# Kernel tuning notes

Measured on AMD Instinct MI355X. Metric: run time of the kernel, lower is better.

## Reference

```python
import jax, jax.numpy as jnp
import numpy as np

B, N, C = 2, 2048, 256
L, H = 4, 4
HD = C // H  # 64, div=1 so q/k keep full head dim
EPS = 1e-5   # BatchNorm eps (eval mode, running_mean=0, running_var=1)


def setup_inputs() -> dict:
    key = jax.random.key(0)
    ks = jax.random.split(key, 20)
    w = lambda k, s: jax.random.normal(k, s, jnp.float32) * 0.05
    return {
        'x': jax.random.normal(ks[0], (B, N, C), jnp.float32),
        'in_w1': w(ks[1], (C, C)), 'in_b1': w(ks[2], (C,)),
        'in_g1': 1.0 + w(ks[3], (C,)), 'in_be1': w(ks[4], (C,)),
        'in_w2': w(ks[5], (C, C)), 'in_b2': w(ks[6], (C,)),
        'in_g2': 1.0 + w(ks[7], (C,)), 'in_be2': w(ks[8], (C,)),
        'q_w': w(ks[9], (L, H, HD, HD)), 'k_w': w(ks[10], (L, H, HD, HD)),
        'v_w': w(ks[11], (L, H, HD, HD)), 'v_b': w(ks[12], (L, H, HD)),
        't_w': w(ks[13], (L, H, HD, HD)), 't_b': w(ks[14], (L, H, HD)),
        'bn_g': 1.0 + w(ks[15], (L, H, HD)), 'bn_b': w(ks[16], (L, H, HD)),
        'proj_w': w(ks[17], (L, C, C)), 'proj_b': w(ks[18], (L, C)),
    }


def _bn(t, g, b):
    # eval-mode BatchNorm1d with running_mean=0, running_var=1
    return t * (g / jnp.sqrt(1.0 + EPS))[:, None] + b[:, None]


def _forward(x, in_w1, in_b1, in_g1, in_be1, in_w2, in_b2, in_g2, in_be2,
             q_w, k_w, v_w, v_b, t_w, t_b, bn_g, bn_b, proj_w, proj_b):
    Bq, Nq, Cq = x.shape
    h = x.transpose(0, 2, 1)  # (B, C, N)
    h = jax.nn.relu(_bn(jnp.einsum('oc,bcn->bon', in_w1, h) + in_b1[:, None], in_g1, in_be1))
    h = jax.nn.relu(_bn(jnp.einsum('oc,bcn->bon', in_w2, h) + in_b2[:, None], in_g2, in_be2))
    h = h.reshape(Bq, H, HD, Nq)  # split heads (B, H, hd, N)
    for l in range(L):
        xq = jnp.einsum('hoc,bhcn->bhno', q_w[l], h)                       # (B,H,N,hd)
        xk = jnp.einsum('hoc,bhcn->bhon', k_w[l], h)                       # (B,H,hd,N)
        xv = jnp.einsum('hoc,bhcn->bhon', v_w[l], h) + v_b[l][None, :, :, None]
        attn = jax.nn.softmax(jnp.einsum('bhno,bhom->bhnm', xq, xk), axis=-1)
        # offset-attention normalization: divide by column sums (torch dim=1)
        attn = attn / (1e-9 + attn.sum(axis=2, keepdims=True))
        xr = jnp.einsum('bhcn,bhnm->bhcm', xv, attn)                       # (B,H,hd,N)
        d = h - xr
        t = jnp.einsum('hoc,bhcn->bhon', t_w[l], d) + t_b[l][None, :, :, None]
        xr = jax.nn.relu(t * (bn_g[l] / jnp.sqrt(1.0 + EPS))[None, :, :, None]
                         + bn_b[l][None, :, :, None])
        h = h + xr
        hm = h.reshape(Bq, Cq, Nq)  # concat heads
        hm = jnp.einsum('oc,bcn->bon', proj_w[l], hm) + proj_b[l][:, None]
        h = hm.reshape(Bq, H, HD, Nq)
    return h.reshape(Bq, Cq, Nq).transpose(0, 2, 1)  # (B, N, C)


def reference(x, in_w1, in_b1, in_g1, in_be1, in_w2, in_b2, in_g2, in_be2,
              q_w, k_w, v_w, v_b, t_w, t_b, bn_g, bn_b, proj_w, proj_b):
    return _forward(x, in_w1, in_b1, in_g1, in_be1, in_w2, in_b2, in_g2, in_be2,
                    q_w, k_w, v_w, v_b, t_w, t_b, bn_g, bn_b, proj_w, proj_b)
```

## Files before the change

kernel.cpp:

```cpp
#include <hip/hip_runtime.h>
#include <math.h>

constexpr int NB = 2, NN = 2048, NC = 256, NL = 4, NH = 4, ND = 64;
constexpr float EPSV = 1e-5f;

using half8 = __attribute__((ext_vector_type(8))) _Float16;
using half4 = __attribute__((ext_vector_type(4))) _Float16;
using f32x4 = __attribute__((ext_vector_type(4))) float;

__device__ __forceinline__ f32x4 mfma16(half8 a, half8 b, f32x4 c) {
    return __builtin_amdgcn_mfma_f32_16x16x32_f16(a, b, c, 0, 0, 0);
}
__device__ __forceinline__ half8 cvt8(const float* p) {
    float4 x0 = *(const float4*)p, x1 = *(const float4*)(p + 4);
    half8 h;
    h[0]=(_Float16)x0.x; h[1]=(_Float16)x0.y; h[2]=(_Float16)x0.z; h[3]=(_Float16)x0.w;
    h[4]=(_Float16)x1.x; h[5]=(_Float16)x1.y; h[6]=(_Float16)x1.z; h[7]=(_Float16)x1.w;
    return h;
}

template<int EPI, bool INF16, bool OUT32>
__global__ __launch_bounds__(256) void gemm_mfma(
    const float* __restrict__ Wg, const float* __restrict__ bias,
    const float* __restrict__ gam, const float* __restrict__ bet,
    const void* __restrict__ inp, void* __restrict__ outp)
{
    int b = blockIdx.x, o0 = blockIdx.y * 64, n0 = blockIdx.z * 32;
    int t = threadIdx.x, w = t >> 6, li = t & 15, qd = (t >> 4) & 3;
    const float* wr = Wg + (size_t)(o0 + w * 16 + li) * NC + qd * 8;
    half8 af[8];
#pragma unroll
    for (int ks = 0; ks < 8; ++ks) af[ks] = cvt8(wr + ks * 32);
    f32x4 acc[2];
    acc[0] = {0.f, 0.f, 0.f, 0.f}; acc[1] = {0.f, 0.f, 0.f, 0.f};
#pragma unroll
    for (int ks = 0; ks < 8; ++ks) {
#pragma unroll
        for (int g = 0; g < 2; ++g) {
            int n = n0 + g * 16 + li;
            half8 bf;
            if (INF16) {
                bf = *(const half8*)((const _Float16*)inp +
                        ((size_t)(b * NN + n) * NC + ks * 32 + qd * 8));
            } else {
                bf = cvt8((const float*)inp + ((size_t)(b * NN + n) * NC + ks * 32 + qd * 8));
            }
            acc[g] = mfma16(af[ks], bf, acc[g]);
        }
    }
    int ob = o0 + w * 16 + qd * 4;
    float4 bs = *(const float4*)(bias + ob);
    float4 gs = {0,0,0,0}, be = {0,0,0,0};
    if (EPI == 1) { gs = *(const float4*)(gam + ob); be = *(const float4*)(bet + ob); }
    float scl = rsqrtf(1.f + EPSV);
#pragma unroll
    for (int g = 0; g < 2; ++g) {
        int n = n0 + g * 16 + li;
        float v4[4];
#pragma unroll
        for (int r = 0; r < 4; ++r) {
            float v = acc[g][r] + ((const float*)&bs)[r];
            if (EPI == 1)
                v = fmaxf(0.f, v * (((const float*)&gs)[r] * scl) + ((const float*)&be)[r]);
            v4[r] = v;
        }
        if (OUT32) {
            float4 fv = {v4[0], v4[1], v4[2], v4[3]};
            *(float4*)((float*)outp + (size_t)(b * NN + n) * NC + ob) = fv;
        } else {
            half4 hv;
#pragma unroll
            for (int r = 0; r < 4; ++r) hv[r] = (_Float16)v4[r];
            *(half4*)((_Float16*)outp + (size_t)(b * NN + n) * NC + ob) = hv;
        }
    }
}

__global__ __launch_bounds__(256) void qkv_fused(
    const float* __restrict__ qw, const float* __restrict__ kw,
    const float* __restrict__ vw, const float* __restrict__ vb,
    const _Float16* __restrict__ h16, _Float16* __restrict__ q16,
    _Float16* __restrict__ k16, _Float16* __restrict__ v16, int l)
{
    int bh = blockIdx.x, n0 = blockIdx.y * 64;
    int hh = bh & 3, b = bh >> 2;
    size_t wbase = (size_t)(l * NH + hh) * ND * ND;
    int t = threadIdx.x, w = t >> 6, li = t & 15, qd = (t >> 4) & 3;
    size_t wro = (size_t)(w * 16 + li) * ND + qd * 8;
    half8 aq0 = cvt8(qw + wbase + wro), aq1 = cvt8(qw + wbase + wro + 32);
    half8 ak0 = cvt8(kw + wbase + wro), ak1 = cvt8(kw + wbase + wro + 32);
    half8 av0 = cvt8(vw + wbase + wro), av1 = cvt8(vw + wbase + wro + 32);
    f32x4 accq[4], acck[4], accv[4];
#pragma unroll
    for (int g = 0; g < 4; ++g) {
        accq[g] = {0.f,0.f,0.f,0.f}; acck[g] = {0.f,0.f,0.f,0.f}; accv[g] = {0.f,0.f,0.f,0.f};
    }
#pragma unroll
    for (int g = 0; g < 4; ++g) {
        int n = n0 + g * 16 + li;
        const _Float16* hb = h16 + ((size_t)(b * NN + n) * NC + hh * 64 + qd * 8);
        half8 b0 = *(const half8*)(hb);
        half8 b1 = *(const half8*)(hb + 32);
        accq[g] = mfma16(aq0, b0, accq[g]); accq[g] = mfma16(aq1, b1, accq[g]);
        acck[g] = mfma16(ak0, b0, acck[g]); acck[g] = mfma16(ak1, b1, acck[g]);
        accv[g] = mfma16(av0, b0, accv[g]); accv[g] = mfma16(av1, b1, accv[g]);
    }
    int ob = w * 16 + qd * 4;
    _Float16* qo = q16 + (size_t)bh * NN * ND;
    _Float16* ko = k16 + (size_t)bh * NN * ND;
#pragma unroll
    for (int g = 0; g < 4; ++g) {
        int n = n0 + g * 16 + li;
        half4 hq, hk;
#pragma unroll
        for (int r = 0; r < 4; ++r) { hq[r] = (_Float16)accq[g][r]; hk[r] = (_Float16)acck[g][r]; }
        *(half4*)(qo + (size_t)n * ND + ob) = hq;
        *(half4*)(ko + (size_t)n * ND + ob) = hk;
    }
    float4 vb4 = *(const float4*)(vb + (size_t)(l * NH + hh) * ND + ob);
    _Float16* vo = v16 + (size_t)bh * ND * NN;
#pragma unroll
    for (int g = 0; g < 4; ++g) {
        int n = n0 + g * 16 + li;
#pragma unroll
        for (int r = 0; r < 4; ++r)
            vo[(size_t)(ob + r) * NN + n] = (_Float16)(accv[g][r] + ((const float*)&vb4)[r]);
    }
}

__global__ __launch_bounds__(256) void rowsum_part(
    const _Float16* __restrict__ qh, const _Float16* __restrict__ kh,
    float* __restrict__ rowsum_p)
{
    int bh = blockIdx.x, nt = blockIdx.y, ms = blockIdx.z;
    const _Float16* qp = qh + (size_t)bh * NN * ND;
    const _Float16* kp = kh + (size_t)bh * NN * ND;
    int t = threadIdx.x, w = t >> 6, li = t & 15, qd = (t >> 4) & 3;
    int nr = nt * 64 + w * 16;
    half8 aq0 = *(const half8*)(qp + (size_t)(nr + li) * ND + qd * 8);
    half8 aq1 = *(const half8*)(qp + (size_t)(nr + li) * ND + qd * 8 + 32);
    float rsacc[4] = {0.f, 0.f, 0.f, 0.f};
    for (int it = 0; it < 8; ++it) {
        int m0 = ms * 512 + it * 64;
        f32x4 s[4];
#pragma unroll
        for (int g = 0; g < 4; ++g) {
            const _Float16* kb = kp + (size_t)(m0 + g * 16 + li) * ND + qd * 8;
            half8 b0 = *(const half8*)(kb);
            half8 b1 = *(const half8*)(kb + 32);
            s[g] = {0.f, 0.f, 0.f, 0.f};
            s[g] = mfma16(aq0, b0, s[g]);
            s[g] = mfma16(aq1, b1, s[g]);
        }
#pragma unroll
        for (int r = 0; r < 4; ++r)
            rsacc[r] += __expf(s[0][r]) + __expf(s[1][r]) + __expf(s[2][r]) + __expf(s[3][r]);
    }
#pragma unroll
    for (int r = 0; r < 4; ++r) {
        float v = rsacc[r];
        v += __shfl_xor(v, 1); v += __shfl_xor(v, 2);
        v += __shfl_xor(v, 4); v += __shfl_xor(v, 8);
        if (li == 0) rowsum_p[((size_t)(ms * NB * NH + bh)) * NN + nr + qd * 4 + r] = v;
    }
}

__global__ __launch_bounds__(256) void attn_part(
    const _Float16* __restrict__ qh, const _Float16* __restrict__ kh,
    const _Float16* __restrict__ vh, const float* __restrict__ rowsum_p,
    _Float16* __restrict__ xrp16, float* __restrict__ csp)
{
    int bh = blockIdx.x, m0 = blockIdx.y * 64, ns = blockIdx.z;
    const _Float16* qp = qh + (size_t)bh * NN * ND;
    const _Float16* kp = kh + (size_t)bh * NN * ND;
    const _Float16* vp = vh + (size_t)bh * ND * NN;
    __shared__ __align__(16) _Float16 Plds[2][64 * 72];
    __shared__ float cs_wave[4][64];
    int t = threadIdx.x, w = t >> 6, li = t & 15, qd = (t >> 4) & 3;
    const size_t RSS = (size_t)NB * NH * NN;
    half8 bk[4][2];
#pragma unroll
    for (int g = 0; g < 4; ++g) {
        const _Float16* kb = kp + (size_t)(m0 + g * 16 + li) * ND + qd * 8;
        bk[g][0] = *(const half8*)(kb);
        bk[g][1] = *(const half8*)(kb + 32);
    }
    f32x4 acc[4];
#pragma unroll
    for (int g = 0; g < 4; ++g) acc[g] = {0.f, 0.f, 0.f, 0.f};
    float csacc[4] = {0.f, 0.f, 0.f, 0.f};
    int nb0 = ns * 512;
    const _Float16* qrow0 = qp + (size_t)(nb0 + w * 16 + li) * ND + qd * 8;
    half8 aq0 = *(const half8*)(qrow0);
    half8 aq1 = *(const half8*)(qrow0 + 32);
    int ridx = bh * NN + nb0 + w * 16 + qd * 4;
    float4 r0 = *(const float4*)(rowsum_p + ridx);
    float4 r1 = *(const float4*)(rowsum_p + RSS + ridx);
    float4 r2 = *(const float4*)(rowsum_p + 2 * RSS + ridx);
    float4 r3 = *(const float4*)(rowsum_p + 3 * RSS + ridx);
    for (int it = 0; it < 8; ++it) {
        int n0 = ns * 512 + it * 64;
        _Float16* Pb = Plds[it & 1];
        const _Float16* vrow = vp + (size_t)(w * 16 + li) * NN + n0 + qd * 8;
        half8 av0 = *(const half8*)(vrow);
        half8 av1 = *(const half8*)(vrow + 32);
        f32x4 s[4];
#pragma unroll
        for (int g = 0; g < 4; ++g) {
            s[g] = {0.f, 0.f, 0.f, 0.f};
            s[g] = mfma16(aq0, bk[g][0], s[g]);
            s[g] = mfma16(aq1, bk[g][1], s[g]);
        }
        float irs[4];
        irs[0] = 1.f / (r0.x + r1.x + r2.x + r3.x);
        irs[1] = 1.f / (r0.y + r1.y + r2.y + r3.y);
        irs[2] = 1.f / (r0.z + r1.z + r2.z + r3.z);
        irs[3] = 1.f / (r0.w + r1.w + r2.w + r3.w);
        if (it < 7) {
            const _Float16* nqrow = qp + (size_t)(n0 + 64 + w * 16 + li) * ND + qd * 8;
            aq0 = *(const half8*)(nqrow);
            aq1 = *(const half8*)(nqrow + 32);
            int nridx = bh * NN + n0 + 64 + w * 16 + qd * 4;
            r0 = *(const float4*)(rowsum_p + nridx);
            r1 = *(const float4*)(rowsum_p + RSS + nridx);
            r2 = *(const float4*)(rowsum_p + 2 * RSS + nridx);
            r3 = *(const float4*)(rowsum_p + 3 * RSS + nridx);
        }
#pragma unroll
        for (int g = 0; g < 4; ++g) {
            half4 pv; float lsum = 0.f;
#pragma unroll
            for (int r = 0; r < 4; ++r) {
                float p = __expf(s[g][r]) * irs[r];
                lsum += p;
                pv[r] = (_Float16)p;
            }
            csacc[g] += lsum;
            *(half4*)(&Pb[(g * 16 + li) * 72 + w * 16 + qd * 4]) = pv;
        }
        __syncthreads();
#pragma unroll
        for (int g = 0; g < 4; ++g) {
            half8 b0 = *(const half8*)(&Pb[(g * 16 + li) * 72 + qd * 8]);
            half8 b1 = *(const half8*)(&Pb[(g * 16 + li) * 72 + qd * 8 + 32]);
            acc[g] = mfma16(av0, b0, acc[g]);
            acc[g] = mfma16(av1, b1, acc[g]);
        }
    }
#pragma unroll
    for (int g = 0; g < 4; ++g) {
        float v = csacc[g];
        v += __shfl_xor(v, 16); v += __shfl_xor(v, 32);
        if (qd == 0) cs_wave[w][g * 16 + li] = v;
    }
    __syncthreads();
    if (t < 64) {
        float cs = cs_wave[0][t] + cs_wave[1][t] + cs_wave[2][t] + cs_wave[3][t];
        csp[((size_t)ns * NB * NH + bh) * NN + m0 + t] = cs;
    }
    _Float16* xo = xrp16 + (size_t)ns * ((size_t)NB * NC * NN);
#pragma unroll
    for (int g = 0; g < 4; ++g)
#pragma unroll
        for (int r = 0; r < 4; ++r)
            xo[(size_t)(bh * 64 + w * 16 + qd * 4 + r) * NN + m0 + g * 16 + li] =
                (_Float16)acc[g][r];
}

__global__ __launch_bounds__(256) void delta_fused(
    const float* __restrict__ tw, const float* __restrict__ tb,
    const float* __restrict__ bng, const float* __restrict__ bnb,
    const _Float16* __restrict__ xrp16, const float* __restrict__ csp,
    const _Float16* __restrict__ h16, _Float16* __restrict__ hn16, int l)
{
    int bh = blockIdx.x, n0 = blockIdx.y * 32;
    int hh = bh & 3, b = bh >> 2;
    __shared__ float xt[64][33];
    int t = threadIdx.x;
    {
        int xcol = t & 31, yr = t >> 5;
        int m = n0 + xcol;
        const size_t CSS = (size_t)NB * NH * NN;
        float cs = 1e-9f;
#pragma unroll
        for (int sl = 0; sl < 4; ++sl) cs += csp[sl * CSS + (size_t)bh * NN + m];
        float icv = 1.f / cs;
        const size_t XSS = (size_t)NB * NC * NN;
#pragma unroll
        for (int r = 0; r < 8; ++r) {
            int c = yr + 8 * r;
            size_t off = (size_t)(bh * 64 + c) * NN + m;
            float s = 0.f;
#pragma unroll
            for (int sl = 0; sl < 4; ++sl) s += (float)xrp16[sl * XSS + off];
            xt[c][xcol] = s * icv;
        }
    }
    __syncthreads();
    int w = t >> 6, li = t & 15, qd = (t >> 4) & 3;
    const float* wp = tw + (size_t)(l * NH + hh) * ND * ND;
    const float* wr = wp + (size_t)(w * 16 + li) * ND + qd * 8;
    half8 af0 = cvt8(wr), af1 = cvt8(wr + 32);
    f32x4 acc[2];
    acc[0] = {0.f, 0.f, 0.f, 0.f}; acc[1] = {0.f, 0.f, 0.f, 0.f};
#pragma unroll
    for (int g = 0; g < 2; ++g) {
        int nl = g * 16 + li;
        size_t hoff = (size_t)(b * NN + n0 + nl) * NC + hh * 64;
        half8 h0 = *(const half8*)(h16 + hoff + qd * 8);
        half8 h1 = *(const half8*)(h16 + hoff + 32 + qd * 8);
        half8 b0, b1;
#pragma unroll
        for (int j = 0; j < 8; ++j) {
            b0[j] = (_Float16)((float)h0[j] - xt[qd * 8 + j][nl]);
            b1[j] = (_Float16)((float)h1[j] - xt[32 + qd * 8 + j][nl]);
        }
        acc[g] = mfma16(af0, b0, acc[g]);
        acc[g] = mfma16(af1, b1, acc[g]);
    }
    int ob = w * 16 + qd * 4;
    float4 tb4 = *(const float4*)(tb  + (size_t)(l * NH + hh) * ND + ob);
    float4 g4  = *(const float4*)(bng + (size_t)(l * NH + hh) * ND + ob);
    float4 b4  = *(const float4*)(bnb + (size_t)(l * NH + hh) * ND + ob);
    float scl = rsqrtf(1.f + EPSV);
#pragma unroll
    for (int g = 0; g < 2; ++g) {
        int n = n0 + g * 16 + li;
        size_t off = (size_t)(b * NN + n) * NC + hh * 64 + ob;
        half4 h4 = *(const half4*)(h16 + off);
        half4 hv;
#pragma unroll
        for (int r = 0; r < 4; ++r) {
            float tv = acc[g][r] + ((const float*)&tb4)[r];
            float x2 = fmaxf(0.f, tv * (((const float*)&g4)[r] * scl) + ((const float*)&b4)[r]);
            hv[r] = (_Float16)((float)h4[r] + x2);
        }
        *(half4*)(hn16 + off) = hv;
    }
}

extern "C" void kernel_launch(void* const* d_in, const int* in_sizes, int n_in,
                              void* d_out, int out_size, void* d_ws, size_t ws_size,
                              hipStream_t stream)
{
    (void)in_sizes; (void)n_in; (void)out_size; (void)ws_size;
    const float* x      = (const float*)d_in[0];
    const float* in_w1  = (const float*)d_in[1];
    const float* in_b1  = (const float*)d_in[2];
    const float* in_g1  = (const float*)d_in[3];
    const float* in_be1 = (const float*)d_in[4];
    const float* in_w2  = (const float*)d_in[5];
    const float* in_b2  = (const float*)d_in[6];
    const float* in_g2  = (const float*)d_in[7];
    const float* in_be2 = (const float*)d_in[8];
    const float* q_w    = (const float*)d_in[9];
    const float* k_w    = (const float*)d_in[10];
    const float* v_w    = (const float*)d_in[11];
    const float* v_b    = (const float*)d_in[12];
    const float* t_w    = (const float*)d_in[13];
    const float* t_b    = (const float*)d_in[14];
    const float* bn_g   = (const float*)d_in[15];
    const float* bn_b   = (const float*)d_in[16];
    const float* proj_w = (const float*)d_in[17];
    const float* proj_b = (const float*)d_in[18];

    float* ws = (float*)d_ws;
    const size_t M = (size_t)NB * NC * NN;
    float* rowsum_p = ws;
    float* csp      = ws + 65536;
    _Float16* xrp16 = (_Float16*)(ws + 131072);
    _Float16* hbase = (_Float16*)(ws + 131072 + 2 * M);
    _Float16* h16  = hbase;
    _Float16* hA16 = hbase + M;
    _Float16* q16  = hbase + 2 * M;
    _Float16* k16  = hbase + 3 * M;
    _Float16* v16  = hbase + 4 * M;

    dim3 g1(NB, NC / 64, NN / 32);

    gemm_mfma<1, false, false><<<g1, 256, 0, stream>>>(in_w1, in_b1, in_g1, in_be1, x,    hA16);
    gemm_mfma<1, true,  false><<<g1, 256, 0, stream>>>(in_w2, in_b2, in_g2, in_be2, hA16, h16);

    for (int l = 0; l < NL; l++) {
        qkv_fused<<<dim3(NB * NH, NN / 64), 256, 0, stream>>>(
            q_w, k_w, v_w, v_b, h16, q16, k16, v16, l);
        rowsum_part<<<dim3(NB * NH, NN / 64, 4), 256, 0, stream>>>(q16, k16, rowsum_p);
        attn_part<<<dim3(NB * NH, NN / 64, 4), 256, 0, stream>>>(
            q16, k16, v16, rowsum_p, xrp16, csp);
        delta_fused<<<dim3(NB * NH, NN / 32), 256, 0, stream>>>(
            t_w, t_b, bn_g, bn_b, xrp16, csp, h16, hA16, l);
        if (l < NL - 1) {
            gemm_mfma<0, true, false><<<g1, 256, 0, stream>>>(
                proj_w + (size_t)l * NC * NC, proj_b + (size_t)l * NC,
                nullptr, nullptr, hA16, h16);
        } else {
            gemm_mfma<0, true, true><<<g1, 256, 0, stream>>>(
                proj_w + (size_t)l * NC * NC, proj_b + (size_t)l * NC,
                nullptr, nullptr, hA16, d_out);
        }
    }
}
```

Baseline: 437.6 us.

## Fuse projection GEMM with next layer's QKV projection via shared memory

Replaces the separate projection GEMM and QKV kernel with one kernel. Each block computes one head's 64 output channels for 32 points, writes h16, stages the tile in LDS, then immediately computes Q, K and V from it. This saves one kernel launch per layer and the global re-read of h for QKV. In exchange, each block loads the full 256-wide weight rows into registers, and the block's tile shape differs from the previous GEMM's.

Result: faster. 424.6 us (-3.0%).

```diff
diff --git a/kernel.cpp b/kernel.cpp
--- a/kernel.cpp
+++ b/kernel.cpp
@@ -76,55 +76,107 @@
     }
 }
 
-__global__ __launch_bounds__(256) void qkv_fused(
+template<int EPI, bool FINAL>
+__global__ __launch_bounds__(256) void proj_qkv(
+    const float* __restrict__ Wg, const float* __restrict__ bias,
+    const float* __restrict__ gam, const float* __restrict__ bet,
+    const _Float16* __restrict__ inp,
+    _Float16* __restrict__ h16,
+    float* __restrict__ out32,
     const float* __restrict__ qw, const float* __restrict__ kw,
     const float* __restrict__ vw, const float* __restrict__ vb,
-    const _Float16* __restrict__ h16, _Float16* __restrict__ q16,
-    _Float16* __restrict__ k16, _Float16* __restrict__ v16, int l)
-{
-    int bh = blockIdx.x, n0 = blockIdx.y * 64;
+    _Float16* __restrict__ q16, _Float16* __restrict__ k16,
+    _Float16* __restrict__ v16, int lq)
+{
+    int bh = blockIdx.x, n0 = blockIdx.y * 32;
     int hh = bh & 3, b = bh >> 2;
-    size_t wbase = (size_t)(l * NH + hh) * ND * ND;
+    __shared__ __align__(16) _Float16 hp[32][72];
     int t = threadIdx.x, w = t >> 6, li = t & 15, qd = (t >> 4) & 3;
+
+    const float* wr = Wg + (size_t)(hh * 64 + w * 16 + li) * NC + qd * 8;
+    half8 af[8];
+#pragma unroll
+    for (int ks = 0; ks < 8; ++ks) af[ks] = cvt8(wr + ks * 32);
+    f32x4 acc[2];
+    acc[0] = {0.f, 0.f, 0.f, 0.f}; acc[1] = {0.f, 0.f, 0.f, 0.f};
+#pragma unroll
+    for (int ks = 0; ks < 8; ++ks) {
+#pragma unroll
+        for (int g = 0; g < 2; ++g) {
+            int n = n0 + g * 16 + li;
+            half8 bf = *(const half8*)(inp + ((size_t)(b * NN + n) * NC + ks * 32 + qd * 8));
+            acc[g] = mfma16(af[ks], bf, acc[g]);
+        }
+    }
+    int obl = w * 16 + qd * 4;
+    int ob = hh * 64 + obl;
+    float4 bs = *(const float4*)(bias + ob);
+    float4 gs = {0,0,0,0}, be = {0,0,0,0};
+    if (EPI == 1) { gs = *(const float4*)(gam + ob); be = *(const float4*)(bet + ob); }
+    float scl = rsqrtf(1.f + EPSV);
+#pragma unroll
+    for (int g = 0; g < 2; ++g) {
+        int n = n0 + g * 16 + li;
+        float v4[4];
+#pragma unroll
+        for (int r = 0; r < 4; ++r) {
+            float v = acc[g][r] + ((const float*)&bs)[r];
+            if (EPI == 1)
+                v = fmaxf(0.f, v * (((const float*)&gs)[r] * scl) + ((const float*)&be)[r]);
+            v4[r] = v;
+        }
+        if (FINAL) {
+            float4 fv = {v4[0], v4[1], v4[2], v4[3]};
+            *(float4*)(out32 + (size_t)(b * NN + n) * NC + ob) = fv;
+        } else {
+            half4 hv;
+#pragma unroll
+            for (int r = 0; r < 4; ++r) hv[r] = (_Float16)v4[r];
+            *(half4*)(h16 + (size_t)(b * NN + n) * NC + ob) = hv;
+            *(half4*)(&hp[g * 16 + li][obl]) = hv;
+        }
+    }
+    if (FINAL) return;
+    __syncthreads();
+
+    size_t wbase = (size_t)(lq * NH + hh) * ND * ND;
     size_t wro = (size_t)(w * 16 + li) * ND + qd * 8;
     half8 aq0 = cvt8(qw + wbase + wro), aq1 = cvt8(qw + wbase + wro + 32);
     half8 ak0 = cvt8(kw + wbase + wro), ak1 = cvt8(kw + wbase + wro + 32);
     half8 av0 = cvt8(vw + wbase + wro), av1 = cvt8(vw + wbase + wro + 32);
-    f32x4 accq[4], acck[4], accv[4];
-#pragma unroll
-    for (int g = 0; g < 4; ++g) {
+    f32x4 accq[2], acck[2], accv[2];
+#pragma unroll
+    for (int g = 0; g < 2; ++g) {
         accq[g] = {0.f,0.f,0.f,0.f}; acck[g] = {0.f,0.f,0.f,0.f}; accv[g] = {0.f,0.f,0.f,0.f};
     }
 #pragma unroll
-    for (int g = 0; g < 4; ++g) {
-        int n = n0 + g * 16 + li;
-        const _Float16* hb = h16 + ((size_t)(b * NN + n) * NC + hh * 64 + qd * 8);
-        half8 b0 = *(const half8*)(hb);
-        half8 b1 = *(const half8*)(hb + 32);
+    for (int g = 0; g < 2; ++g) {
+        half8 b0 = *(const half8*)(&hp[g * 16 + li][qd * 8]);
+        half8 b1 = *(const half8*)(&hp[g * 16 + li][qd * 8 + 32]);
         accq[g] = mfma16(aq0, b0, accq[g]); accq[g] = mfma16(aq1, b1, accq[g]);
         acck[g] = mfma16(ak0, b0, acck[g]); acck[g] = mfma16(ak1, b1, acck[g]);
         accv[g] = mfma16(av0, b0, accv[g]); accv[g] = mfma16(av1, b1, accv[g]);
     }
-    int ob = w * 16 + qd * 4;
+    int obq = w * 16 + qd * 4;
     _Float16* qo = q16 + (size_t)bh * NN * ND;
     _Float16* ko = k16 + (size_t)bh * NN * ND;
 #pragma unroll
-    for (int g = 0; g < 4; ++g) {
+    for (int g = 0; g < 2; ++g) {
         int n = n0 + g * 16 + li;
         half4 hq, hk;
 #pragma unroll
         for (int r = 0; r < 4; ++r) { hq[r] = (_Float16)accq[g][r]; hk[r] = (_Float16)acck[g][r]; }
-        *(half4*)(qo + (size_t)n * ND + ob) = hq;
-        *(half4*)(ko + (size_t)n * ND + ob) = hk;
-    }
-    float4 vb4 = *(const float4*)(vb + (size_t)(l * NH + hh) * ND + ob);
+        *(half4*)(qo + (size_t)n * ND + obq) = hq;
+        *(half4*)(ko + (size_t)n * ND + obq) = hk;
+    }
+    float4 vb4 = *(const float4*)(vb + (size_t)(lq * NH + hh) * ND + obq);
     _Float16* vo = v16 + (size_t)bh * ND * NN;
 #pragma unroll
-    for (int g = 0; g < 4; ++g) {
+    for (int g = 0; g < 2; ++g) {
         int n = n0 + g * 16 + li;
 #pragma unroll
         for (int r = 0; r < 4; ++r)
-            vo[(size_t)(ob + r) * NN + n] = (_Float16)(accv[g][r] + ((const float*)&vb4)[r]);
+            vo[(size_t)(obq + r) * NN + n] = (_Float16)(accv[g][r] + ((const float*)&vb4)[r]);
     }
 }
 
@@ -377,26 +429,29 @@
     _Float16* v16  = hbase + 4 * M;
 
     dim3 g1(NB, NC / 64, NN / 32);
-
-    gemm_mfma<1, false, false><<<g1, 256, 0, stream>>>(in_w1, in_b1, in_g1, in_be1, x,    hA16);
-    gemm_mfma<1, true,  false><<<g1, 256, 0, stream>>>(in_w2, in_b2, in_g2, in_be2, hA16, h16);
+    dim3 gf(NB * NH, NN / 32);
+
+    gemm_mfma<1, false, false><<<g1, 256, 0, stream>>>(in_w1, in_b1, in_g1, in_be1, x, hA16);
+    proj_qkv<1, false><<<gf, 256, 0, stream>>>(
+        in_w2, in_b2, in_g2, in_be2, hA16, h16, nullptr,
+        q_w, k_w, v_w, v_b, q16, k16, v16, 0);
 
     for (int l = 0; l < NL; l++) {
-        qkv_fused<<<dim3(NB * NH, NN / 64), 256, 0, stream>>>(
-            q_w, k_w, v_w, v_b, h16, q16, k16, v16, l);
         rowsum_part<<<dim3(NB * NH, NN / 64, 4), 256, 0, stream>>>(q16, k16, rowsum_p);
         attn_part<<<dim3(NB * NH, NN / 64, 4), 256, 0, stream>>>(
             q16, k16, v16, rowsum_p, xrp16, csp);
         delta_fused<<<dim3(NB * NH, NN / 32), 256, 0, stream>>>(
             t_w, t_b, bn_g, bn_b, xrp16, csp, h16, hA16, l);
         if (l < NL - 1) {
-            gemm_mfma<0, true, false><<<g1, 256, 0, stream>>>(
+            proj_qkv<0, false><<<gf, 256, 0, stream>>>(
                 proj_w + (size_t)l * NC * NC, proj_b + (size_t)l * NC,
-                nullptr, nullptr, hA16, h16);
+                nullptr, nullptr, hA16, h16, nullptr,
+                q_w, k_w, v_w, v_b, q16, k16, v16, l + 1);
         } else {
-            gemm_mfma<0, true, true><<<g1, 256, 0, stream>>>(
+            proj_qkv<0, true><<<gf, 256, 0, stream>>>(
                 proj_w + (size_t)l * NC * NC, proj_b + (size_t)l * NC,
-                nullptr, nullptr, hA16, d_out);
-        }
-    }
-}
+                nullptr, nullptr, hA16, nullptr, (float*)d_out,
+                q_w, k_w, v_w, v_b, q16, k16, v16, 0);
+        }
+    }
+}
```
